# Kernel optimization log

Measured on AMD Instinct MI355X. Metric: run time of the kernel, lower is better.

## Reference

```python
import jax, jax.numpy as jnp
import numpy as np

N = 100000      # n_nodes
D = 64          # in_features (= out_features)
H = 4           # attention heads
DK = D // H     # per-head dim
E = 1600000     # num edges (avg degree 16)
STEP = 0.25     # ODE euler step size
NSTEPS = 4      # integrate t in [0, 1]
ALPHA = 0.2     # LeakyReLU negative slope


def setup_inputs() -> dict:
    key = jax.random.key(0)
    k1, k2, k3, k4 = jax.random.split(key, 4)
    x = jax.random.normal(k1, (N, D), dtype=jnp.float32)
    edge_index = jax.random.randint(k2, (2, E), 0, N, dtype=jnp.int32)
    edge_weight = jax.random.uniform(k3, (E,), dtype=jnp.float32)
    # HamAgg.weight: init.eye_ -> identity [D, D]
    W = jnp.eye(D, dtype=jnp.float32)
    # HAM_GATConv.a: xavier_normal_ on shape (2*d_k, 1, 1), gain=1.414
    a = jax.random.normal(k4, (2 * DK,), dtype=jnp.float32) * (1.414 * np.sqrt(2.0 / (2 * DK + 1)))
    return {"x": x, "edge_index": edge_index, "edge_weight": edge_weight, "W": W, "a": a}


def reference(x, edge_index, edge_weight, W, a):
    # ---- Hamiltonian ODE block (args.vt == 'fc', odemap 'h1extend') ----
    # xt = hstack([x, x @ W.T]); euler-integrate canonical Hamiltonian flow
    # dq/dt = p, dp/dt = -q over t in [0,1] with step 0.25; keep first D dims.
    q = x
    p = x @ W.T
    for _ in range(NSTEPS):
        q, p = q + STEP * p, p - STEP * q
    xt = q  # out_x = out[..., :D]

    row, col = edge_index[0], edge_index[1]

    # ---- HAM_GATConv attention (W_x = x @ I = x) ----
    # h[n, head, k] = xt[n, head*DK + k]
    h = xt.reshape(N, H, DK)
    a_src, a_dst = a[:DK], a[DK:]
    s_src = h @ a_src   # [N, H] per-node source contribution
    s_dst = h @ a_dst   # [N, H] per-node dest contribution
    score = jax.nn.leaky_relu(s_src[row] + s_dst[col], ALPHA)  # [E, H]

    # segment softmax grouped by destination (edge[1])
    seg_max = jax.ops.segment_max(score, col, num_segments=N)  # [N, H]
    seg_max = jnp.where(jnp.isfinite(seg_max), seg_max, 0.0)
    e = jnp.exp(score - seg_max[col])
    denom = jax.ops.segment_sum(e, col, num_segments=N)
    att = e / (denom[col] + 1e-16)  # [E, H]

    # ---- mean over heads of per-head spmm == single spmm with mean attention ----
    # spmm: out[row[e]] += att[e] * xt[col[e]]
    w = att.mean(axis=1)  # [E]
    out = jax.ops.segment_sum(w[:, None] * xt[col], row, num_segments=N)  # [N, D]
    return out
```

## Files before the change

### kernel.cpp

```cpp
#include <hip/hip_runtime.h>
#include <hip/hip_bf16.h>


#define LRELU(v) ((v) > 0.0f ? (v) : 0.2f * (v))

#define EC 4096
#define BSC 256
#define BSR 128
#define SLOTS 4

typedef __attribute__((ext_vector_type(8))) short bf16x8;
typedef __attribute__((ext_vector_type(4))) float f32x4;

__device__ __forceinline__ float bf16_to_f32(unsigned short u) {
    return __uint_as_float((unsigned int)u << 16);
}
__device__ __forceinline__ float bflo(unsigned int u) {
    return __uint_as_float(u << 16);
}
__device__ __forceinline__ float bfhi(unsigned int u) {
    return __uint_as_float(u & 0xFFFF0000u);
}
__device__ __forceinline__ unsigned short f32_to_bf16(float f) {
    __hip_bfloat16 h = __float2bfloat16(f);
    return *reinterpret_cast<unsigned short*>(&h);
}

__global__ __launch_bounds__(256) void k_geff(const float* __restrict__ W,
                                              const float* __restrict__ a,
                                              unsigned short* __restrict__ geff16,
                                              float c1, float c2) {
    int t = threadIdx.x;
    int k = t & 63, h = t >> 6;
    float ssrc = 0.0f, sdst = 0.0f;
#pragma unroll
    for (int d = 0; d < 16; ++d) {
        float w = W[(h * 16 + d) * 64 + k];
        ssrc += w * a[d];
        sdst += w * a[16 + d];
    }
    float gsrc = c2 * ssrc, gdst = c2 * sdst;
    if ((k >> 4) == h) {
        gsrc += c1 * a[k & 15];
        gdst += c1 * a[16 + (k & 15)];
    }
    unsigned short sh = f32_to_bf16(gsrc);
    unsigned short sl = f32_to_bf16(gsrc - bf16_to_f32(sh));
    unsigned short dh = f32_to_bf16(gdst);
    unsigned short dl = f32_to_bf16(gdst - bf16_to_f32(dh));
    geff16[h * 64 + k] = sh;
    geff16[(4 + h) * 64 + k] = dh;
    geff16[(8 + h) * 64 + k] = sl;
    geff16[(12 + h) * 64 + k] = dl;
}

__global__ __launch_bounds__(256) void k_node(const float* __restrict__ x,
                                              const float* __restrict__ W,
                                              const unsigned short* __restrict__ geff16,
                                              unsigned short* __restrict__ xt16,
                                              float* __restrict__ s_src,
                                              float* __restrict__ s_dst,
                                              int n, float c1, float c2) {
    int wave = threadIdx.x >> 6;
    int lane = threadIdx.x & 63;
    int nb = blockIdx.x * 64 + wave * 16;
    if (nb >= n) return;
    int colg = lane & 15;
    int grp = lane >> 4;
    int k0 = grp << 3;

    bf16x8 wf[4][2];
#pragma unroll
    for (int ct = 0; ct < 4; ++ct) {
#pragma unroll
        for (int ks = 0; ks < 2; ++ks) {
            const float* wr = W + (size_t)(ct * 16 + colg) * 64 + k0 + ks * 32;
            float4 w0 = *(const float4*)(wr);
            float4 w1 = *(const float4*)(wr + 4);
            bf16x8 f;
            f[0] = (short)f32_to_bf16(w0.x); f[1] = (short)f32_to_bf16(w0.y);
            f[2] = (short)f32_to_bf16(w0.z); f[3] = (short)f32_to_bf16(w0.w);
            f[4] = (short)f32_to_bf16(w1.x); f[5] = (short)f32_to_bf16(w1.y);
            f[6] = (short)f32_to_bf16(w1.z); f[7] = (short)f32_to_bf16(w1.w);
            wf[ct][ks] = f;
        }
    }
    bf16x8 gf[2];
#pragma unroll
    for (int ks = 0; ks < 2; ++ks)
        gf[ks] = *(const bf16x8*)(geff16 + colg * 64 + k0 + ks * 32);

    int arow = nb + colg;
    if (arow >= n) arow = n - 1;
    const float* xr = x + (size_t)arow * 64 + k0;
    bf16x8 af[2];
#pragma unroll
    for (int ks = 0; ks < 2; ++ks) {
        float4 x0 = *(const float4*)(xr + ks * 32);
        float4 x1 = *(const float4*)(xr + ks * 32 + 4);
        bf16x8 f;
        f[0] = (short)f32_to_bf16(x0.x); f[1] = (short)f32_to_bf16(x0.y);
        f[2] = (short)f32_to_bf16(x0.z); f[3] = (short)f32_to_bf16(x0.w);
        f[4] = (short)f32_to_bf16(x1.x); f[5] = (short)f32_to_bf16(x1.y);
        f[6] = (short)f32_to_bf16(x1.z); f[7] = (short)f32_to_bf16(x1.w);
        af[ks] = f;
    }

    f32x4 acc[5];
#pragma unroll
    for (int i = 0; i < 5; ++i) acc[i] = (f32x4){0.f, 0.f, 0.f, 0.f};
#pragma unroll
    for (int ct = 0; ct < 4; ++ct) {
        acc[ct] = __builtin_amdgcn_mfma_f32_16x16x32_bf16(af[0], wf[ct][0], acc[ct], 0, 0, 0);
        acc[ct] = __builtin_amdgcn_mfma_f32_16x16x32_bf16(af[1], wf[ct][1], acc[ct], 0, 0, 0);
    }
    acc[4] = __builtin_amdgcn_mfma_f32_16x16x32_bf16(af[0], gf[0], acc[4], 0, 0, 0);
    acc[4] = __builtin_amdgcn_mfma_f32_16x16x32_bf16(af[1], gf[1], acc[4], 0, 0, 0);

#pragma unroll
    for (int ct = 0; ct < 4; ++ct) {
        int col = ct * 16 + colg;
#pragma unroll
        for (int rr = 0; rr < 4; ++rr) {
            int node = nb + grp * 4 + rr;
            if (node < n) {
                float xv = x[(size_t)node * 64 + col];
                float xtv = c1 * xv + c2 * acc[ct][rr];
                xt16[(size_t)node * 64 + col] = f32_to_bf16(xtv);
            }
        }
    }
#pragma unroll
    for (int rr = 0; rr < 4; ++rr) {
        float v = acc[4][rr];
        float tot = v + __shfl_xor(v, 8, 64);
        int node = nb + grp * 4 + rr;
        if (node < n) {
            if (colg < 4) s_src[node * 4 + colg] = tot;
            else if (colg < 8) s_dst[node * 4 + (colg - 4)] = tot;
        }
    }
}

__global__ __launch_bounds__(256) void k_hist(const int* __restrict__ row,
                                              const int* __restrict__ col,
                                              int* __restrict__ Hr,
                                              int* __restrict__ Hc,
                                              int e, int nblk, int nbr, int nbc) {
    __shared__ int hr[1024];
    __shared__ int hc[512];
    int t = threadIdx.x;
    for (int i = t; i < 1024; i += 256) hr[i] = 0;
    for (int i = t; i < 512; i += 256) hc[i] = 0;
    __syncthreads();
    int base = blockIdx.x * EC;
#pragma unroll
    for (int j = 0; j < EC / 256; ++j) {
        int i = base + t + j * 256;
        if (i < e) {
            atomicAdd(&hr[row[i] >> 7], 1);
            atomicAdd(&hc[col[i] >> 8], 1);
        }
    }
    __syncthreads();
    for (int b = t; b < nbr; b += 256) Hr[(size_t)b * nblk + blockIdx.x] = hr[b];
    for (int b = t; b < nbc; b += 256) Hc[(size_t)b * nblk + blockIdx.x] = hc[b];
}

__global__ __launch_bounds__(256) void k_scanH2(int* __restrict__ Hr,
                                                int* __restrict__ Hc,
                                                int* __restrict__ BtotR,
                                                int* __restrict__ BtotC,
                                                int nblk, int nbr) {
    __shared__ int vals[512];
    __shared__ int part[256];
    int t = threadIdx.x;
    int bb = blockIdx.x;
    int* Hb;
    int* Btot;
    if (bb < nbr) {
        Hb = Hr + (size_t)bb * nblk;
        Btot = BtotR + bb;
    } else {
        Hb = Hc + (size_t)(bb - nbr) * nblk;
        Btot = BtotC + (bb - nbr);
    }
    for (int i = t; i < nblk; i += 256) vals[i] = Hb[i];
    __syncthreads();
    int c0 = t * 2;
    int s = 0;
#pragma unroll
    for (int j = 0; j < 2; ++j)
        if (c0 + j < nblk) s += vals[c0 + j];
    part[t] = s;
    __syncthreads();
    for (int d = 1; d < 256; d <<= 1) {
        int add = (t >= d) ? part[t - d] : 0;
        __syncthreads();
        part[t] += add;
        __syncthreads();
    }
    int run = part[t] - s;
#pragma unroll
    for (int j = 0; j < 2; ++j) {
        int i = c0 + j;
        if (i < nblk) {
            int v = vals[i];
            Hb[i] = run;
            run += v;
        }
    }
    if (t == 255) *Btot = part[255];
}

__global__ __launch_bounds__(256) void k_base2(const int* __restrict__ BtotR,
                                               int* __restrict__ BbR, int nbr,
                                               const int* __restrict__ BtotC,
                                               int* __restrict__ BbC, int nbc) {
    const int* Btot = (blockIdx.x == 0) ? BtotR : BtotC;
    int* Bbase = (blockIdx.x == 0) ? BbR : BbC;
    int nb = (blockIdx.x == 0) ? nbr : nbc;
    __shared__ int part[256];
    __shared__ int carry;
    int t = threadIdx.x;
    if (t == 0) carry = 0;
    __syncthreads();
    for (int base = 0; base < nb; base += 256) {
        int i = base + t;
        int v = (i < nb) ? Btot[i] : 0;
        part[t] = v;
        __syncthreads();
        for (int d = 1; d < 256; d <<= 1) {
            int add = (t >= d) ? part[t - d] : 0;
            __syncthreads();
            part[t] += add;
            __syncthreads();
        }
        if (i < nb) Bbase[i] = carry + part[t] - v;
        __syncthreads();
        if (t == 0) carry += part[255];
        __syncthreads();
    }
    if (t == 0) Bbase[nb] = carry;
}

__global__ __launch_bounds__(256) void k_scatter_dual(
    const int* __restrict__ row, const int* __restrict__ col,
    const int* __restrict__ Hr, const int* __restrict__ Hc,
    const int* __restrict__ BbR, const int* __restrict__ BbC,
    int* __restrict__ ebr, int* __restrict__ ebc,
    int e, int nblk, int nbr, int nbc) {
    __shared__ int curr[1024];
    __shared__ int curc[512];
    int t = threadIdx.x;
    int blk = blockIdx.x;
    for (int b = t; b < nbr; b += 256) curr[b] = BbR[b] + Hr[(size_t)b * nblk + blk];
    for (int b = t; b < nbc; b += 256) curc[b] = BbC[b] + Hc[(size_t)b * nblk + blk];
    __syncthreads();
    int base = blk * EC;
#pragma unroll
    for (int j = 0; j < EC / 256; ++j) {
        int i = base + t + j * 256;
        if (i < e) {
            int r = row[i], c = col[i];
            int pr = atomicAdd(&curr[r >> 7], 1);
            ebr[pr] = (c << 7) | (r & 127);
            int pc = atomicAdd(&curc[c >> 8], 1);
            ebc[pc] = (r << 8) | (c & 255);
        }
    }
}

__global__ __launch_bounds__(256) void k_denom_b(const int* __restrict__ ebc,
                                                 const int* __restrict__ BbC,
                                                 const float* __restrict__ s_src,
                                                 const float* __restrict__ s_dst,
                                                 float* __restrict__ rden, int n) {
    __shared__ float acc[BSC * 4];
    __shared__ float sd[BSC * 4];
    int t = threadIdx.x;
    int b = blockIdx.x;
    int cbase = b << 8;
    for (int i = t; i < BSC * 4; i += 256) {
        acc[i] = 0.0f;
        int c4 = cbase * 4 + i;
        sd[i] = (c4 < n * 4) ? s_dst[c4] : 0.0f;
    }
    __syncthreads();
    int start = BbC[b], end = BbC[b + 1];
    for (int i = start + t; i < end; i += 256) {
        int p = ebc[i];
        int r = p >> 8, cl = p & 255;
        float4 ss = *(const float4*)(s_src + (size_t)r * 4);
        atomicAdd(&acc[cl * 4 + 0], __expf(LRELU(ss.x + sd[cl * 4 + 0])));
        atomicAdd(&acc[cl * 4 + 1], __expf(LRELU(ss.y + sd[cl * 4 + 1])));
        atomicAdd(&acc[cl * 4 + 2], __expf(LRELU(ss.z + sd[cl * 4 + 2])));
        atomicAdd(&acc[cl * 4 + 3], __expf(LRELU(ss.w + sd[cl * 4 + 3])));
    }
    __syncthreads();
    for (int i = t; i < BSC * 4; i += 256) {
        int c4 = cbase * 4 + i;
        if (c4 < n * 4) rden[c4] = 1.0f / (acc[i] + 1e-16f);
    }
}

__global__ __launch_bounds__(256) void k_sort2(const int* __restrict__ ebr,
                                               const int* __restrict__ BbR,
                                               const float* __restrict__ s_src,
                                               const float* __restrict__ s_dst,
                                               const float* __restrict__ rden,
                                               int* __restrict__ rowptr,
                                               int2* __restrict__ cwp,
                                               int n, int e) {
    __shared__ int cnt[BSR];
    __shared__ int pfx[BSR];
    __shared__ int cur[BSR];
    __shared__ float ssh[BSR * 4];
    int t = threadIdx.x;
    int b = blockIdx.x;
    int rbase = b << 7;
    if (t < BSR) cnt[t] = 0;
    for (int i = t; i < BSR * 4; i += 256) {
        int g = rbase * 4 + i;
        ssh[i] = (g < n * 4) ? s_src[g] : 0.0f;
    }
    __syncthreads();
    int start = BbR[b], end = BbR[b + 1];
    for (int i = start + t; i < end; i += 256)
        atomicAdd(&cnt[ebr[i] & 127], 1);
    __syncthreads();
    if (t < BSR) pfx[t] = cnt[t];
    __syncthreads();
    for (int d = 1; d < BSR; d <<= 1) {
        int v = (t < BSR && t >= d) ? pfx[t - d] : 0;
        __syncthreads();
        if (t < BSR) pfx[t] += v;
        __syncthreads();
    }
    if (t < BSR) {
        int excl = start + pfx[t] - cnt[t];
        cur[t] = excl;
        int r = rbase + t;
        if (r < n) rowptr[r] = excl;
    }
    if (b == 0 && t == 0) rowptr[n] = e;
    __syncthreads();
    for (int i = start + t; i < end; i += 256) {
        int p = ebr[i];
        int rl = p & 127, c = p >> 7;
        float4 sd = *(const float4*)(s_dst + (size_t)c * 4);
        float4 rd = *(const float4*)(rden + (size_t)c * 4);
        float wv = __expf(LRELU(ssh[rl * 4 + 0] + sd.x)) * rd.x +
                   __expf(LRELU(ssh[rl * 4 + 1] + sd.y)) * rd.y +
                   __expf(LRELU(ssh[rl * 4 + 2] + sd.z)) * rd.z +
                   __expf(LRELU(ssh[rl * 4 + 3] + sd.w)) * rd.w;
        int pos = atomicAdd(&cur[rl], 1);
        cwp[pos] = make_int2(c << 6, __float_as_int(0.25f * wv));
    }
}

__global__ __launch_bounds__(256) void k_aggr(const int* __restrict__ rowptr,
                                              const int2* __restrict__ cwp,
                                              const unsigned short* __restrict__ xt16,
                                              float* __restrict__ out, int n, int e) {
    int r = blockIdx.x * 4 + (threadIdx.x >> 6);
    if (r >= n) return;
    int lane = threadIdx.x & 63;
    int g = lane >> 3;
    unsigned le = (lane & 7) << 3;
    int start = rowptr[r], end = rowptr[r + 1];
    float acc[8];
#pragma unroll
    for (int j = 0; j < 8; ++j) acc[j] = 0.0f;
    for (int base = start; base < end; base += SLOTS * 8) {
        int m = end - base;
        if (m > SLOTS * 8) m = SLOTS * 8;
        int nk = (m + 7) >> 3;
        uint4 u[SLOTS];
        float wv[SLOTS];
#pragma unroll
        for (int k = 0; k < SLOTS; ++k) {
            if (k < nk) {
                int idx = base + k * 8 + g;
                int idc = idx < e ? idx : e - 1;
                int2 cw = cwp[idc];
                wv[k] = (idx < end) ? __int_as_float(cw.y) : 0.0f;
                u[k] = *(const uint4*)(xt16 + ((unsigned)cw.x + le));
            }
        }
#pragma unroll
        for (int k = 0; k < SLOTS; ++k) {
            if (k < nk) {
                acc[0] = fmaf(wv[k], bflo(u[k].x), acc[0]);
                acc[1] = fmaf(wv[k], bfhi(u[k].x), acc[1]);
                acc[2] = fmaf(wv[k], bflo(u[k].y), acc[2]);
                acc[3] = fmaf(wv[k], bfhi(u[k].y), acc[3]);
                acc[4] = fmaf(wv[k], bflo(u[k].z), acc[4]);
                acc[5] = fmaf(wv[k], bfhi(u[k].z), acc[5]);
                acc[6] = fmaf(wv[k], bflo(u[k].w), acc[6]);
                acc[7] = fmaf(wv[k], bfhi(u[k].w), acc[7]);
            }
        }
    }
#pragma unroll
    for (int off = 8; off <= 32; off <<= 1) {
#pragma unroll
        for (int j = 0; j < 8; ++j) acc[j] += __shfl_xor(acc[j], off, 64);
    }
    if (lane < 8) {
        float4 a0 = {acc[0], acc[1], acc[2], acc[3]};
        float4 a1 = {acc[4], acc[5], acc[6], acc[7]};
        *(float4*)(out + (size_t)r * 64 + le) = a0;
        *(float4*)(out + (size_t)r * 64 + le + 4) = a1;
    }
}

extern "C" void kernel_launch(void* const* d_in, const int* in_sizes, int n_in,
                              void* d_out, int out_size, void* d_ws, size_t ws_size,
                              hipStream_t stream) {
    const float* x = (const float*)d_in[0];
    const int* ei = (const int*)d_in[1];
    const float* W = (const float*)d_in[3];
    const float* a = (const float*)d_in[4];
    int n = in_sizes[0] / 64;
    int e = in_sizes[1] / 2;
    const int* row = ei;
    const int* col = ei + e;
    float* out = (float*)d_out;

    int nblk = (e + EC - 1) / EC;
    int nbr = (n + BSR - 1) / BSR;
    int nbc = (n + BSC - 1) / BSC;

    size_t o = 0;
    auto take = [&](size_t cnt) {
        size_t p = o;
        o += (cnt + 3) & ~(size_t)3;
        return p;
    };
    int* wsi = (int*)d_ws;
    unsigned short* xt16 = (unsigned short*)(wsi + take((size_t)n * 32));
    float* s_src = (float*)(wsi + take((size_t)n * 4));
    float* s_dst = (float*)(wsi + take((size_t)n * 4));
    float* rden = (float*)(wsi + take((size_t)n * 4));
    unsigned short* geff16 = (unsigned short*)(wsi + take(512));
    int* Hr = wsi + take((size_t)nbr * nblk);
    int* Hc = wsi + take((size_t)nbc * nblk);
    int* BtotR = wsi + take(nbr);
    int* BbR = wsi + take(nbr + 1);
    int* BtotC = wsi + take(nbc);
    int* BbC = wsi + take(nbc + 1);
    int* ebr = wsi + take(e);
    int* cwbuf = wsi + take((size_t)2 * e);
    int* ebc = cwbuf;
    int2* cwp = (int2*)cwbuf;
    int* rowptr = wsi + take(n + 1);

    float aq = 1.f, bq = 0.f, ap = 0.f, bp = 1.f;
    for (int i = 0; i < 4; ++i) {
        float naq = aq + 0.25f * ap, nbq = bq + 0.25f * bp;
        float nap = ap - 0.25f * aq, nbp = bp - 0.25f * bq;
        aq = naq; bq = nbq; ap = nap; bp = nbp;
    }

    k_geff<<<1, 256, 0, stream>>>(W, a, geff16, aq, bq);
    k_node<<<(n + 63) / 64, 256, 0, stream>>>(x, W, geff16, xt16, s_src, s_dst,
                                              n, aq, bq);
    k_hist<<<nblk, 256, 0, stream>>>(row, col, Hr, Hc, e, nblk, nbr, nbc);
    k_scanH2<<<nbr + nbc, 256, 0, stream>>>(Hr, Hc, BtotR, BtotC, nblk, nbr);
    k_base2<<<2, 256, 0, stream>>>(BtotR, BbR, nbr, BtotC, BbC, nbc);
    k_scatter_dual<<<nblk, 256, 0, stream>>>(row, col, Hr, Hc, BbR, BbC,
                                             ebr, ebc, e, nblk, nbr, nbc);
    k_denom_b<<<nbc, 256, 0, stream>>>(ebc, BbC, s_src, s_dst, rden, n);
    k_sort2<<<nbr, 256, 0, stream>>>(ebr, BbR, s_src, s_dst, rden,
                                     rowptr, cwp, n, e);
    k_aggr<<<(n + 3) / 4, 256, 0, stream>>>(rowptr, cwp, xt16, out, n, e);
}
```

Before: 300.8 us.

## Replace column bucket sort for softmax denominators with direct global atomics

Drops the column-side histogram, scan and scatter passes that bucketed edges by destination. Softmax denominators are now built by one edge-parallel kernel that does global float atomicAdds into a per-node buffer, which is zeroed in the node kernel. The sort kernel divides by the denominator per edge instead of multiplying by a precomputed reciprocal. This removes a full edge scatter and its memory traffic, but adds 6.4M global atomics with random addresses and extra divides.

```diff
diff --git a/kernel.cpp b/kernel.cpp
--- a/kernel.cpp
+++ b/kernel.cpp
@@ -5,7 +5,6 @@
 #define LRELU(v) ((v) > 0.0f ? (v) : 0.2f * (v))
 
 #define EC 4096
-#define BSC 256
 #define BSR 128
 #define SLOTS 4
 
@@ -60,6 +59,7 @@
                                               unsigned short* __restrict__ xt16,
                                               float* __restrict__ s_src,
                                               float* __restrict__ s_dst,
+                                              float* __restrict__ den,
                                               int n, float c1, float c2) {
     int wave = threadIdx.x >> 6;
     int lane = threadIdx.x & 63;
@@ -138,53 +138,35 @@
         if (node < n) {
             if (colg < 4) s_src[node * 4 + colg] = tot;
             else if (colg < 8) s_dst[node * 4 + (colg - 4)] = tot;
+            else if (colg < 12) den[node * 4 + (colg - 8)] = 0.0f;
         }
     }
 }
 
 __global__ __launch_bounds__(256) void k_hist(const int* __restrict__ row,
-                                              const int* __restrict__ col,
                                               int* __restrict__ Hr,
-                                              int* __restrict__ Hc,
-                                              int e, int nblk, int nbr, int nbc) {
+                                              int e, int nblk, int nbr) {
     __shared__ int hr[1024];
-    __shared__ int hc[512];
     int t = threadIdx.x;
     for (int i = t; i < 1024; i += 256) hr[i] = 0;
-    for (int i = t; i < 512; i += 256) hc[i] = 0;
     __syncthreads();
     int base = blockIdx.x * EC;
 #pragma unroll
     for (int j = 0; j < EC / 256; ++j) {
         int i = base + t + j * 256;
-        if (i < e) {
-            atomicAdd(&hr[row[i] >> 7], 1);
-            atomicAdd(&hc[col[i] >> 8], 1);
-        }
+        if (i < e) atomicAdd(&hr[row[i] >> 7], 1);
     }
     __syncthreads();
     for (int b = t; b < nbr; b += 256) Hr[(size_t)b * nblk + blockIdx.x] = hr[b];
-    for (int b = t; b < nbc; b += 256) Hc[(size_t)b * nblk + blockIdx.x] = hc[b];
-}
-
-__global__ __launch_bounds__(256) void k_scanH2(int* __restrict__ Hr,
-                                                int* __restrict__ Hc,
-                                                int* __restrict__ BtotR,
-                                                int* __restrict__ BtotC,
-                                                int nblk, int nbr) {
+}
+
+__global__ __launch_bounds__(256) void k_scanH(int* __restrict__ Hr,
+                                               int* __restrict__ BtotR,
+                                               int nblk) {
     __shared__ int vals[512];
     __shared__ int part[256];
     int t = threadIdx.x;
-    int bb = blockIdx.x;
-    int* Hb;
-    int* Btot;
-    if (bb < nbr) {
-        Hb = Hr + (size_t)bb * nblk;
-        Btot = BtotR + bb;
-    } else {
-        Hb = Hc + (size_t)(bb - nbr) * nblk;
-        Btot = BtotC + (bb - nbr);
-    }
+    int* Hb = Hr + (size_t)blockIdx.x * nblk;
     for (int i = t; i < nblk; i += 256) vals[i] = Hb[i];
     __syncthreads();
     int c0 = t * 2;
@@ -210,16 +192,11 @@
             run += v;
         }
     }
-    if (t == 255) *Btot = part[255];
-}
-
-__global__ __launch_bounds__(256) void k_base2(const int* __restrict__ BtotR,
-                                               int* __restrict__ BbR, int nbr,
-                                               const int* __restrict__ BtotC,
-                                               int* __restrict__ BbC, int nbc) {
-    const int* Btot = (blockIdx.x == 0) ? BtotR : BtotC;
-    int* Bbase = (blockIdx.x == 0) ? BbR : BbC;
-    int nb = (blockIdx.x == 0) ? nbr : nbc;
+    if (t == 255) BtotR[blockIdx.x] = part[255];
+}
+
+__global__ __launch_bounds__(256) void k_base(const int* __restrict__ BtotR,
+                                              int* __restrict__ BbR, int nb) {
     __shared__ int part[256];
     __shared__ int carry;
     int t = threadIdx.x;
@@ -227,7 +204,7 @@
     __syncthreads();
     for (int base = 0; base < nb; base += 256) {
         int i = base + t;
-        int v = (i < nb) ? Btot[i] : 0;
+        int v = (i < nb) ? BtotR[i] : 0;
         part[t] = v;
         __syncthreads();
         for (int d = 1; d < 256; d <<= 1) {
@@ -236,26 +213,22 @@
             part[t] += add;
             __syncthreads();
         }
-        if (i < nb) Bbase[i] = carry + part[t] - v;
+        if (i < nb) BbR[i] = carry + part[t] - v;
         __syncthreads();
         if (t == 0) carry += part[255];
         __syncthreads();
     }
-    if (t == 0) Bbase[nb] = carry;
-}
-
-__global__ __launch_bounds__(256) void k_scatter_dual(
+    if (t == 0) BbR[nb] = carry;
+}
+
+__global__ __launch_bounds__(256) void k_scatter(
     const int* __restrict__ row, const int* __restrict__ col,
-    const int* __restrict__ Hr, const int* __restrict__ Hc,
-    const int* __restrict__ BbR, const int* __restrict__ BbC,
-    int* __restrict__ ebr, int* __restrict__ ebc,
-    int e, int nblk, int nbr, int nbc) {
+    const int* __restrict__ Hr, const int* __restrict__ BbR,
+    int* __restrict__ ebr, int e, int nblk, int nbr) {
     __shared__ int curr[1024];
-    __shared__ int curc[512];
     int t = threadIdx.x;
     int blk = blockIdx.x;
     for (int b = t; b < nbr; b += 256) curr[b] = BbR[b] + Hr[(size_t)b * nblk + blk];
-    for (int b = t; b < nbc; b += 256) curc[b] = BbC[b] + Hc[(size_t)b * nblk + blk];
     __syncthreads();
     int base = blk * EC;
 #pragma unroll
@@ -265,42 +238,45 @@
             int r = row[i], c = col[i];
             int pr = atomicAdd(&curr[r >> 7], 1);
             ebr[pr] = (c << 7) | (r & 127);
-            int pc = atomicAdd(&curc[c >> 8], 1);
-            ebc[pc] = (r << 8) | (c & 255);
-        }
-    }
-}
-
-__global__ __launch_bounds__(256) void k_denom_b(const int* __restrict__ ebc,
-                                                 const int* __restrict__ BbC,
+        }
+    }
+}
+
+__global__ __launch_bounds__(256) void k_denom_e(const int* __restrict__ row,
+                                                 const int* __restrict__ col,
                                                  const float* __restrict__ s_src,
                                                  const float* __restrict__ s_dst,
-                                                 float* __restrict__ rden, int n) {
-    __shared__ float acc[BSC * 4];
-    __shared__ float sd[BSC * 4];
-    int t = threadIdx.x;
-    int b = blockIdx.x;
-    int cbase = b << 8;
-    for (int i = t; i < BSC * 4; i += 256) {
-        acc[i] = 0.0f;
-        int c4 = cbase * 4 + i;
-        sd[i] = (c4 < n * 4) ? s_dst[c4] : 0.0f;
-    }
-    __syncthreads();
-    int start = BbC[b], end = BbC[b + 1];
-    for (int i = start + t; i < end; i += 256) {
-        int p = ebc[i];
-        int r = p >> 8, cl = p & 255;
-        float4 ss = *(const float4*)(s_src + (size_t)r * 4);
-        atomicAdd(&acc[cl * 4 + 0], __expf(LRELU(ss.x + sd[cl * 4 + 0])));
-        atomicAdd(&acc[cl * 4 + 1], __expf(LRELU(ss.y + sd[cl * 4 + 1])));
-        atomicAdd(&acc[cl * 4 + 2], __expf(LRELU(ss.z + sd[cl * 4 + 2])));
-        atomicAdd(&acc[cl * 4 + 3], __expf(LRELU(ss.w + sd[cl * 4 + 3])));
-    }
-    __syncthreads();
-    for (int i = t; i < BSC * 4; i += 256) {
-        int c4 = cbase * 4 + i;
-        if (c4 < n * 4) rden[c4] = 1.0f / (acc[i] + 1e-16f);
+                                                 float* __restrict__ den, int e) {
+    int i0 = (blockIdx.x * 256 + (int)threadIdx.x) * 4;
+    if (i0 + 4 <= e) {
+        int4 r4 = *(const int4*)(row + i0);
+        int4 c4 = *(const int4*)(col + i0);
+        int rr[4] = {r4.x, r4.y, r4.z, r4.w};
+        int cc[4] = {c4.x, c4.y, c4.z, c4.w};
+        float4 ss[4], sd[4];
+#pragma unroll
+        for (int j = 0; j < 4; ++j) ss[j] = *(const float4*)(s_src + (size_t)rr[j] * 4);
+#pragma unroll
+        for (int j = 0; j < 4; ++j) sd[j] = *(const float4*)(s_dst + (size_t)cc[j] * 4);
+#pragma unroll
+        for (int j = 0; j < 4; ++j) {
+            float* d = den + (size_t)cc[j] * 4;
+            atomicAdd(d + 0, __expf(LRELU(ss[j].x + sd[j].x)));
+            atomicAdd(d + 1, __expf(LRELU(ss[j].y + sd[j].y)));
+            atomicAdd(d + 2, __expf(LRELU(ss[j].z + sd[j].z)));
+            atomicAdd(d + 3, __expf(LRELU(ss[j].w + sd[j].w)));
+        }
+    } else {
+        for (int i = i0; i < e; ++i) {
+            int r = row[i], c = col[i];
+            float4 ss = *(const float4*)(s_src + (size_t)r * 4);
+            float4 sd = *(const float4*)(s_dst + (size_t)c * 4);
+            float* d = den + (size_t)c * 4;
+            atomicAdd(d + 0, __expf(LRELU(ss.x + sd.x)));
+            atomicAdd(d + 1, __expf(LRELU(ss.y + sd.y)));
+            atomicAdd(d + 2, __expf(LRELU(ss.z + sd.z)));
+            atomicAdd(d + 3, __expf(LRELU(ss.w + sd.w)));
+        }
     }
 }
 
@@ -308,7 +284,7 @@
                                                const int* __restrict__ BbR,
                                                const float* __restrict__ s_src,
                                                const float* __restrict__ s_dst,
-                                               const float* __restrict__ rden,
+                                               const float* __restrict__ den,
                                                int* __restrict__ rowptr,
                                                int2* __restrict__ cwp,
                                                int n, int e) {
@@ -349,11 +325,11 @@
         int p = ebr[i];
         int rl = p & 127, c = p >> 7;
         float4 sd = *(const float4*)(s_dst + (size_t)c * 4);
-        float4 rd = *(const float4*)(rden + (size_t)c * 4);
-        float wv = __expf(LRELU(ssh[rl * 4 + 0] + sd.x)) * rd.x +
-                   __expf(LRELU(ssh[rl * 4 + 1] + sd.y)) * rd.y +
-                   __expf(LRELU(ssh[rl * 4 + 2] + sd.z)) * rd.z +
-                   __expf(LRELU(ssh[rl * 4 + 3] + sd.w)) * rd.w;
+        float4 rd = *(const float4*)(den + (size_t)c * 4);
+        float wv = __expf(LRELU(ssh[rl * 4 + 0] + sd.x)) / (rd.x + 1e-16f) +
+                   __expf(LRELU(ssh[rl * 4 + 1] + sd.y)) / (rd.y + 1e-16f) +
+                   __expf(LRELU(ssh[rl * 4 + 2] + sd.z)) / (rd.z + 1e-16f) +
+                   __expf(LRELU(ssh[rl * 4 + 3] + sd.w)) / (rd.w + 1e-16f);
         int pos = atomicAdd(&cur[rl], 1);
         cwp[pos] = make_int2(c << 6, __float_as_int(0.25f * wv));
     }
@@ -430,7 +406,6 @@
 
     int nblk = (e + EC - 1) / EC;
     int nbr = (n + BSR - 1) / BSR;
-    int nbc = (n + BSC - 1) / BSC;
 
     size_t o = 0;
     auto take = [&](size_t cnt) {
@@ -442,18 +417,13 @@
     unsigned short* xt16 = (unsigned short*)(wsi + take((size_t)n * 32));
     float* s_src = (float*)(wsi + take((size_t)n * 4));
     float* s_dst = (float*)(wsi + take((size_t)n * 4));
-    float* rden = (float*)(wsi + take((size_t)n * 4));
+    float* den = (float*)(wsi + take((size_t)n * 4));
     unsigned short* geff16 = (unsigned short*)(wsi + take(512));
     int* Hr = wsi + take((size_t)nbr * nblk);
-    int* Hc = wsi + take((size_t)nbc * nblk);
     int* BtotR = wsi + take(nbr);
     int* BbR = wsi + take(nbr + 1);
-    int* BtotC = wsi + take(nbc);
-    int* BbC = wsi + take(nbc + 1);
     int* ebr = wsi + take(e);
-    int* cwbuf = wsi + take((size_t)2 * e);
-    int* ebc = cwbuf;
-    int2* cwp = (int2*)cwbuf;
+    int2* cwp = (int2*)(wsi + take((size_t)2 * e));
     int* rowptr = wsi + take(n + 1);
 
     float aq = 1.f, bq = 0.f, ap = 0.f, bp = 1.f;
@@ -465,14 +435,14 @@
 
     k_geff<<<1, 256, 0, stream>>>(W, a, geff16, aq, bq);
     k_node<<<(n + 63) / 64, 256, 0, stream>>>(x, W, geff16, xt16, s_src, s_dst,
-                                              n, aq, bq);
-    k_hist<<<nblk, 256, 0, stream>>>(row, col, Hr, Hc, e, nblk, nbr, nbc);
-    k_scanH2<<<nbr + nbc, 256, 0, stream>>>(Hr, Hc, BtotR, BtotC, nblk, nbr);
-    k_base2<<<2, 256, 0, stream>>>(BtotR, BbR, nbr, BtotC, BbC, nbc);
-    k_scatter_dual<<<nblk, 256, 0, stream>>>(row, col, Hr, Hc, BbR, BbC,
-                                             ebr, ebc, e, nblk, nbr, nbc);
-    k_denom_b<<<nbc, 256, 0, stream>>>(ebc, BbC, s_src, s_dst, rden, n);
-    k_sort2<<<nbr, 256, 0, stream>>>(ebr, BbR, s_src, s_dst, rden,
+                                              den, n, aq, bq);
+    k_hist<<<nblk, 256, 0, stream>>>(row, Hr, e, nblk, nbr);
+    k_scanH<<<nbr, 256, 0, stream>>>(Hr, BtotR, nblk);
+    k_base<<<1, 256, 0, stream>>>(BtotR, BbR, nbr);
+    k_scatter<<<nblk, 256, 0, stream>>>(row, col, Hr, BbR, ebr, e, nblk, nbr);
+    k_denom_e<<<(e / 4 + 255) / 256, 256, 0, stream>>>(row, col, s_src, s_dst,
+                                                       den, e);
+    k_sort2<<<nbr, 256, 0, stream>>>(ebr, BbR, s_src, s_dst, den,
                                      rowptr, cwp, n, e);
     k_aggr<<<(n + 3) / 4, 256, 0, stream>>>(rowptr, cwp, xt16, out, n, e);
 }
```

New measurement: 570.2 us. +89.6%, slower.

## Split denominator kernel across four slices per bucket and interleave dst score with reciprocal

Applied to the files above, without the earlier changes.

The per-destination-bucket softmax denominator kernel now runs four blocks per bucket, each summing a quarter of the bucket's edges into its own partial buffer. A new combine kernel adds the partials, takes the reciprocal, and writes it interleaved with s_dst into one 8-float record per node. The sort kernel then reads both values from the same cache line. The aim is more parallelism, since there were only ~391 blocks on a large GPU, and fewer scattered loads in the sort pass. The cost is an extra launch and extra partial-buffer traffic.

```diff
diff --git a/kernel.cpp b/kernel.cpp
--- a/kernel.cpp
+++ b/kernel.cpp
@@ -7,6 +7,7 @@
 #define EC 4096
 #define BSC 256
 #define BSR 128
+#define DS 4
 #define SLOTS 4
 
 typedef __attribute__((ext_vector_type(8))) short bf16x8;
@@ -271,24 +272,29 @@
     }
 }
 
-__global__ __launch_bounds__(256) void k_denom_b(const int* __restrict__ ebc,
+__global__ __launch_bounds__(256) void k_denom_p(const int* __restrict__ ebc,
                                                  const int* __restrict__ BbC,
                                                  const float* __restrict__ s_src,
                                                  const float* __restrict__ s_dst,
-                                                 float* __restrict__ rden, int n) {
+                                                 float* __restrict__ part,
+                                                 int n, int n4) {
     __shared__ float acc[BSC * 4];
     __shared__ float sd[BSC * 4];
     int t = threadIdx.x;
-    int b = blockIdx.x;
-    int cbase = b << 8;
+    int bucket = blockIdx.x >> 2;
+    int slice = blockIdx.x & 3;
+    int cbase = bucket << 8;
     for (int i = t; i < BSC * 4; i += 256) {
         acc[i] = 0.0f;
         int c4 = cbase * 4 + i;
-        sd[i] = (c4 < n * 4) ? s_dst[c4] : 0.0f;
-    }
-    __syncthreads();
-    int start = BbC[b], end = BbC[b + 1];
-    for (int i = start + t; i < end; i += 256) {
+        sd[i] = (c4 < n4) ? s_dst[c4] : 0.0f;
+    }
+    __syncthreads();
+    int start = BbC[bucket], end = BbC[bucket + 1];
+    int len = end - start;
+    int i0 = start + (int)(((long long)len * slice) >> 2);
+    int i1 = start + (int)(((long long)len * (slice + 1)) >> 2);
+    for (int i = i0 + t; i < i1; i += 256) {
         int p = ebc[i];
         int r = p >> 8, cl = p & 255;
         float4 ss = *(const float4*)(s_src + (size_t)r * 4);
@@ -298,17 +304,29 @@
         atomicAdd(&acc[cl * 4 + 3], __expf(LRELU(ss.w + sd[cl * 4 + 3])));
     }
     __syncthreads();
+    float* ps = part + (size_t)slice * n4;
     for (int i = t; i < BSC * 4; i += 256) {
         int c4 = cbase * 4 + i;
-        if (c4 < n * 4) rden[c4] = 1.0f / (acc[i] + 1e-16f);
-    }
+        if (c4 < n4) ps[c4] = acc[i];
+    }
+}
+
+__global__ __launch_bounds__(256) void k_comb(const float* __restrict__ part,
+                                              const float* __restrict__ s_dst,
+                                              float* __restrict__ sdr, int n4) {
+    int idx = blockIdx.x * 256 + threadIdx.x;
+    if (idx >= n4) return;
+    float s = part[idx] + part[(size_t)n4 + idx] + part[(size_t)2 * n4 + idx] +
+              part[(size_t)3 * n4 + idx];
+    int c = idx >> 2, h = idx & 3;
+    sdr[(size_t)c * 8 + h] = s_dst[idx];
+    sdr[(size_t)c * 8 + 4 + h] = 1.0f / (s + 1e-16f);
 }
 
 __global__ __launch_bounds__(256) void k_sort2(const int* __restrict__ ebr,
                                                const int* __restrict__ BbR,
                                                const float* __restrict__ s_src,
-                                               const float* __restrict__ s_dst,
-                                               const float* __restrict__ rden,
+                                               const float* __restrict__ sdr,
                                                int* __restrict__ rowptr,
                                                int2* __restrict__ cwp,
                                                int n, int e) {
@@ -348,8 +366,8 @@
     for (int i = start + t; i < end; i += 256) {
         int p = ebr[i];
         int rl = p & 127, c = p >> 7;
-        float4 sd = *(const float4*)(s_dst + (size_t)c * 4);
-        float4 rd = *(const float4*)(rden + (size_t)c * 4);
+        float4 sd = *(const float4*)(sdr + (size_t)c * 8);
+        float4 rd = *(const float4*)(sdr + (size_t)c * 8 + 4);
         float wv = __expf(LRELU(ssh[rl * 4 + 0] + sd.x)) * rd.x +
                    __expf(LRELU(ssh[rl * 4 + 1] + sd.y)) * rd.y +
                    __expf(LRELU(ssh[rl * 4 + 2] + sd.z)) * rd.z +
@@ -431,6 +449,7 @@
     int nblk = (e + EC - 1) / EC;
     int nbr = (n + BSR - 1) / BSR;
     int nbc = (n + BSC - 1) / BSC;
+    int n4 = n * 4;
 
     size_t o = 0;
     auto take = [&](size_t cnt) {
@@ -442,7 +461,8 @@
     unsigned short* xt16 = (unsigned short*)(wsi + take((size_t)n * 32));
     float* s_src = (float*)(wsi + take((size_t)n * 4));
     float* s_dst = (float*)(wsi + take((size_t)n * 4));
-    float* rden = (float*)(wsi + take((size_t)n * 4));
+    float* sdr = (float*)(wsi + take((size_t)n * 8));
+    float* part = (float*)(wsi + take((size_t)n * 4 * DS));
     unsigned short* geff16 = (unsigned short*)(wsi + take(512));
     int* Hr = wsi + take((size_t)nbr * nblk);
     int* Hc = wsi + take((size_t)nbc * nblk);
@@ -471,8 +491,8 @@
     k_base2<<<2, 256, 0, stream>>>(BtotR, BbR, nbr, BtotC, BbC, nbc);
     k_scatter_dual<<<nblk, 256, 0, stream>>>(row, col, Hr, Hc, BbR, BbC,
                                              ebr, ebc, e, nblk, nbr, nbc);
-    k_denom_b<<<nbc, 256, 0, stream>>>(ebc, BbC, s_src, s_dst, rden, n);
-    k_sort2<<<nbr, 256, 0, stream>>>(ebr, BbR, s_src, s_dst, rden,
-                                     rowptr, cwp, n, e);
+    k_denom_p<<<nbc * DS, 256, 0, stream>>>(ebc, BbC, s_src, s_dst, part, n, n4);
+    k_comb<<<(n4 + 255) / 256, 256, 0, stream>>>(part, s_dst, sdr, n4);
+    k_sort2<<<nbr, 256, 0, stream>>>(ebr, BbR, s_src, sdr, rowptr, cwp, n, e);
     k_aggr<<<(n + 3) / 4, 256, 0, stream>>>(rowptr, cwp, xt16, out, n, e);
 }
```

Result: faster. 288.8 us (-4.0%).
